# Performance work log

Measured on AMD Instinct MI355X. Metric: run time of the kernel, lower is better.

Reference implementation:

```python
import jax, jax.numpy as jnp
import numpy as np

B, N, E = 4, 2048, 512
H, DK, DV = 8, 64, 64
QKV_OUT = H * (2 * DK + DV)  # 1536


def setup_inputs() -> dict:
    key = jax.random.key(0)
    ks = jax.random.split(key, 5)
    s_in = 1.0 / np.sqrt(E)
    s_o = 1.0 / np.sqrt(H * DV)
    x = jax.random.normal(ks[0], (B, N, E), dtype=jnp.float32)
    W_qkv = jax.random.uniform(ks[1], (E, QKV_OUT), jnp.float32, -s_in, s_in)
    b_qkv = jax.random.uniform(ks[2], (QKV_OUT,), jnp.float32, -s_in, s_in)
    W_o = jax.random.uniform(ks[3], (H * DV, E), jnp.float32, -s_o, s_o)
    b_o = jax.random.uniform(ks[4], (E,), jnp.float32, -s_o, s_o)
    return {"x": x, "W_qkv": W_qkv, "b_qkv": b_qkv, "W_o": W_o, "b_o": b_o}


def reference(x, W_qkv, b_qkv, W_o, b_o):
    scale = DK ** (-0.5)
    qkv = x @ W_qkv + b_qkv                      # [B, N, H*(2dk+dv)]
    # Faithful to torch: raw view (B, H, N, 2dk+dv), NOT a head-split transpose.
    qkv = qkv.reshape(B, H, N, 2 * DK + DV)
    q = qkv[..., :DK]
    k = qkv[..., DK:2 * DK]
    v = qkv[..., 2 * DK:]
    # Faithful bug: qk /= scale with scale = dk^-0.5 -> multiply by sqrt(dk).
    qk = jnp.einsum('bhnd,bhmd->bhnm', q, k) / scale   # [B, H, N, N]
    attn = jax.nn.softmax(qk, axis=-1)
    y = jnp.einsum('bhnm,bhmd->bhnd', attn, v)         # [B, H, N, dv]
    y = y.reshape(B, N, H * DV)
    return y @ W_o + b_o
```

## Files before the change

kernel.cpp:

```cpp
#include <hip/hip_runtime.h>
#include <hip/hip_bf16.h>
#include <math.h>


typedef __attribute__((ext_vector_type(8))) short bf16x8;
typedef __attribute__((ext_vector_type(4))) float f32x4;

#define MFMA16(a, b, c) __builtin_amdgcn_mfma_f32_16x16x32_bf16((a), (b), (c), 0, 0, 0)

__device__ __forceinline__ ushort f2bf_rne(float f) {
  union { float f; unsigned u; } v; v.f = f;
  return (ushort)((v.u + 0x7fffu + ((v.u >> 16) & 1u)) >> 16);
}
__device__ __forceinline__ float bf2f(ushort h) {
  union { float f; unsigned u; } v; v.u = ((unsigned)h) << 16; return v.f;
}
__device__ __forceinline__ void split2(float f, ushort& hi, ushort& lo) {
  union { float f; unsigned u; } v; v.f = f;
  hi = (ushort)(v.u >> 16);
  union { float f; unsigned u; } r; r.f = f - bf2f(hi);
  lo = (ushort)(r.u >> 16);
}

__global__ __launch_bounds__(256) void cvtw_k(const float* __restrict__ wqkv,
                                              const float* __restrict__ wo,
                                              ushort* __restrict__ wT_hi,
                                              ushort* __restrict__ wT_lo,
                                              ushort* __restrict__ woT)
{
  const int gid = blockIdx.x * 256 + threadIdx.x;
  if (gid < 786432) {
    const int n = gid >> 9, k = gid & 511;
    ushort hi, lo; split2(wqkv[(size_t)k * 1536 + n], hi, lo);
    wT_hi[gid] = hi; wT_lo[gid] = lo;
  } else {
    const int g = gid - 786432;
    const int n = g >> 9, k = g & 511;
    woT[g] = f2bf_rne(wo[(size_t)k * 512 + n]);
  }
}

__global__ __launch_bounds__(256) void cvtx_k(const float* __restrict__ x,
                                              ushort* __restrict__ xh,
                                              ushort* __restrict__ xl)
{
  const int gid = blockIdx.x * 256 + threadIdx.x;
  float4 v = ((const float4*)x)[gid];
  ushort4 hh, ll;
  split2(v.x, hh.x, ll.x); split2(v.y, hh.y, ll.y);
  split2(v.z, hh.z, ll.z); split2(v.w, hh.w, ll.w);
  ((ushort4*)xh)[gid] = hh;
  ((ushort4*)xl)[gid] = ll;
}

template <bool PRECVT>
__global__ __launch_bounds__(256) void qkv_gemm_k(
    const float* __restrict__ x,
    const ushort* __restrict__ xh, const ushort* __restrict__ xl,
    const ushort* __restrict__ wT_hi, const ushort* __restrict__ wT_lo,
    const float* __restrict__ bqkv,
    ushort* __restrict__ q_hi, ushort* __restrict__ q_lo,
    ushort* __restrict__ k_hi, ushort* __restrict__ k_lo,
    ushort* __restrict__ v_nat)
{
  const int i = blockIdx.x, j = i >> 3;
  const int tmb = (i & 7) * 8 + (j & 7);
  const int tn  = j >> 3;
  const int tid = threadIdx.x, lane = tid & 63, w = tid >> 6;
  const int col16 = lane & 15, quad = lane >> 4;
  const int wr = w >> 1, wc = w & 1;

  __shared__ short bh_lds[2][128][40];
  __shared__ short bl_lds[2][128][40];

  const int sn = tid >> 1, sk = (tid & 1) * 16;
  const ushort* bhsrc = wT_hi + (size_t)(tn * 128 + sn) * 512 + sk;
  const ushort* blsrc = wT_lo + (size_t)(tn * 128 + sn) * 512 + sk;

  const float*  axf[4];
  const ushort *axh[4], *axl[4];
#pragma unroll
  for (int rt = 0; rt < 4; ++rt) {
    const size_t rowoff = (size_t)(tmb * 128 + wr * 64 + rt * 16 + col16) * 512 + quad * 8;
    axf[rt] = x  + rowoff;
    axh[rt] = xh + rowoff;
    axl[rt] = xl + rowoff;
  }

  f32x4 acc[4][4];
#pragma unroll
  for (int rt = 0; rt < 4; ++rt)
#pragma unroll
    for (int ct = 0; ct < 4; ++ct) acc[rt][ct] = (f32x4){0.f, 0.f, 0.f, 0.f};

  uint4 rb0 = *(const uint4*)(bhsrc);
  uint4 rb1 = *(const uint4*)(bhsrc + 8);
  uint4 rb2 = *(const uint4*)(blsrc);
  uint4 rb3 = *(const uint4*)(blsrc + 8);
  *(uint4*)(&bh_lds[0][sn][sk])     = rb0;
  *(uint4*)(&bh_lds[0][sn][sk + 8]) = rb1;
  *(uint4*)(&bl_lds[0][sn][sk])     = rb2;
  *(uint4*)(&bl_lds[0][sn][sk + 8]) = rb3;

  for (int c = 0; c < 16; ++c) {
    __syncthreads();
    if (c < 15) {
      const int k0 = (c + 1) * 32;
      rb0 = *(const uint4*)(bhsrc + k0);
      rb1 = *(const uint4*)(bhsrc + k0 + 8);
      rb2 = *(const uint4*)(blsrc + k0);
      rb3 = *(const uint4*)(blsrc + k0 + 8);
    }
    const int b = c & 1, k0 = c * 32;

    bf16x8 bh[4], bl[4];
#pragma unroll
    for (int ct = 0; ct < 4; ++ct) {
      bh[ct] = *(const bf16x8*)(&bh_lds[b][wc * 64 + ct * 16 + col16][quad * 8]);
      bl[ct] = *(const bf16x8*)(&bl_lds[b][wc * 64 + ct * 16 + col16][quad * 8]);
    }
#pragma unroll
    for (int rt = 0; rt < 4; ++rt) {
      bf16x8 a_hi, a_lo;
      if constexpr (PRECVT) {
        a_hi = *(const bf16x8*)(axh[rt] + k0);
        a_lo = *(const bf16x8*)(axl[rt] + k0);
      } else {
        float4 xa = *(const float4*)(axf[rt] + k0);
        float4 xb = *(const float4*)(axf[rt] + k0 + 4);
#pragma unroll
        for (int jj = 0; jj < 4; ++jj) {
          ushort h, l;
          split2(((const float*)&xa)[jj], h, l);
          ((short*)&a_hi)[jj] = (short)h; ((short*)&a_lo)[jj] = (short)l;
          split2(((const float*)&xb)[jj], h, l);
          ((short*)&a_hi)[4 + jj] = (short)h; ((short*)&a_lo)[4 + jj] = (short)l;
        }
      }
#pragma unroll
      for (int ct = 0; ct < 4; ++ct) {
        acc[rt][ct] = MFMA16(a_hi, bh[ct], acc[rt][ct]);
        acc[rt][ct] = MFMA16(a_hi, bl[ct], acc[rt][ct]);
        acc[rt][ct] = MFMA16(a_lo, bh[ct], acc[rt][ct]);
      }
    }
    if (c < 15) {
      const int nb = b ^ 1;
      *(uint4*)(&bh_lds[nb][sn][sk])     = rb0;
      *(uint4*)(&bh_lds[nb][sn][sk + 8]) = rb1;
      *(uint4*)(&bl_lds[nb][sn][sk])     = rb2;
      *(uint4*)(&bl_lds[nb][sn][sk + 8]) = rb3;
    }
  }

  short* eph = ((short*)bh_lds) + w * 1152;
  short* epl = ((short*)bl_lds) + w * 1152;
  const int g0   = tn * 128 + wc * 64;
  const int sect = (g0 % 192) >> 6;
  const int s    = g0 / 192;
  float bv[4];
#pragma unroll
  for (int ct = 0; ct < 4; ++ct) bv[ct] = bqkv[g0 + ct * 16 + col16];

#pragma unroll
  for (int rt = 0; rt < 4; ++rt) {
#pragma unroll
    for (int ct = 0; ct < 4; ++ct) {
#pragma unroll
      for (int r = 0; r < 4; ++r) {
        const float val = acc[rt][ct][r] + bv[ct];
        const int o = (quad * 4 + r) * 72 + ct * 16 + col16;
        if (sect == 2) {
          eph[o] = (short)f2bf_rne(val);
        } else {
          ushort h, l; split2(val, h, l);
          eph[o] = (short)h; epl[o] = (short)l;
        }
      }
    }
#pragma unroll
    for (int p = 0; p < 2; ++p) {
      const int row = p * 8 + (lane >> 3);
      const int dsg = (lane & 7) * 8;
      const int grow = tmb * 128 + wr * 64 + rt * 16 + row;
      const int bhh = grow >> 8, a = grow & 255;
      const size_t idx = ((size_t)bhh * 2048 + 8 * a + s) * 64 + dsg;
      uint4 hv = *(const uint4*)(eph + row * 72 + dsg);
      if (sect == 0) {
        *(uint4*)(q_hi + idx) = hv;
        uint4 lv = *(const uint4*)(epl + row * 72 + dsg);
        *(uint4*)(q_lo + idx) = lv;
      } else if (sect == 1) {
        *(uint4*)(k_hi + idx) = hv;
        uint4 lv = *(const uint4*)(epl + row * 72 + dsg);
        *(uint4*)(k_lo + idx) = lv;
      } else {
        *(uint4*)(v_nat + idx) = hv;
      }
    }
  }
}

__global__ __launch_bounds__(256) void vtrans_k(const ushort* __restrict__ v_nat,
                                                ushort* __restrict__ vT)
{
  const int t  = blockIdx.x & 7;
  const int bh = blockIdx.x >> 3;
  const int tid = threadIdx.x;
  const int nl = tid & 63;
  const int dg = tid >> 6;
  const size_t base = (size_t)bh * 2048 * 64;
#pragma unroll
  for (int p = 0; p < 2; ++p) {
    const int dseg = dg + p * 4;
#pragma unroll
    for (int nb = 0; nb < 4; ++nb) {
      const int n = t * 256 + nb * 64 + nl;
      uint4 vv = *(const uint4*)(v_nat + base + (size_t)n * 64 + dseg * 8);
      const ushort* pv = (const ushort*)&vv;
#pragma unroll
      for (int j = 0; j < 8; ++j)
        vT[base + (size_t)(dseg * 8 + j) * 2048 + n] = pv[j];
    }
  }
}

__global__ __launch_bounds__(256, 2) void attn_k(
    const ushort* __restrict__ q_hi, const ushort* __restrict__ q_lo,
    const ushort* __restrict__ k_hi, const ushort* __restrict__ k_lo,
    const ushort* __restrict__ vT, ushort* __restrict__ y)
{
  const int i  = blockIdx.x;
  const int bh = (i & 7) * 4 + (i >> 7);
  const int qt = (i >> 3) & 15;
  const int tid = threadIdx.x, lane = tid & 63, w = tid >> 6;
  const int col16 = lane & 15, quad = lane >> 4;

  __shared__ short kh_lds[2][64][72], kl_lds[2][64][72], vt_lds[2][64][72];
  __shared__ short p_lds[4][2][16][72];

  const size_t base = (size_t)bh * 2048 * 64;
  const int qw = qt * 128 + w * 32;

  bf16x8 qh[2][2], ql[2][2];
#pragma unroll
  for (int rf = 0; rf < 2; ++rf)
#pragma unroll
    for (int ks = 0; ks < 2; ++ks) {
      const size_t off = base + (size_t)(qw + rf * 16 + col16) * 64 + ks * 32 + quad * 8;
      qh[rf][ks] = *(const bf16x8*)(q_hi + off);
      ql[rf][ks] = *(const bf16x8*)(q_lo + off);
    }

  f32x4 oacc[2][4];
#pragma unroll
  for (int rf = 0; rf < 2; ++rf)
#pragma unroll
    for (int ct = 0; ct < 4; ++ct) oacc[rf][ct] = (f32x4){0.f, 0.f, 0.f, 0.f};
  f32x4 lsum[2] = {(f32x4){0.f, 0.f, 0.f, 0.f}, (f32x4){0.f, 0.f, 0.f, 0.f}};

  const int sn = tid >> 2, sd = (tid & 3) * 16;
  const ushort* khsrc = k_hi + base + (size_t)sn * 64 + sd;
  const ushort* klsrc = k_lo + base + (size_t)sn * 64 + sd;
  const ushort* vtsrc = vT  + base + (size_t)sn * 2048 + sd;

  const float S2 = 11.541560327111707f;

  uint4 r0 = *(const uint4*)(khsrc);
  uint4 r1 = *(const uint4*)(khsrc + 8);
  uint4 r2 = *(const uint4*)(klsrc);
  uint4 r3 = *(const uint4*)(klsrc + 8);
  uint4 r4 = *(const uint4*)(vtsrc);
  uint4 r5 = *(const uint4*)(vtsrc + 8);
  *(uint4*)(&kh_lds[0][sn][sd])     = r0;
  *(uint4*)(&kh_lds[0][sn][sd + 8]) = r1;
  *(uint4*)(&kl_lds[0][sn][sd])     = r2;
  *(uint4*)(&kl_lds[0][sn][sd + 8]) = r3;
  *(uint4*)(&vt_lds[0][sn][sd])     = r4;
  *(uint4*)(&vt_lds[0][sn][sd + 8]) = r5;

  for (int c = 0; c < 32; ++c) {
    __syncthreads();
    if (c < 31) {
      const size_t ko = (size_t)(c + 1) * 4096;
      r0 = *(const uint4*)(khsrc + ko);
      r1 = *(const uint4*)(khsrc + ko + 8);
      r2 = *(const uint4*)(klsrc + ko);
      r3 = *(const uint4*)(klsrc + ko + 8);
      r4 = *(const uint4*)(vtsrc + (c + 1) * 64);
      r5 = *(const uint4*)(vtsrc + (c + 1) * 64 + 8);
    }
    const int b = c & 1;

    f32x4 sacc[2][4];
#pragma unroll
    for (int rf = 0; rf < 2; ++rf)
#pragma unroll
      for (int ct = 0; ct < 4; ++ct) sacc[rf][ct] = (f32x4){0.f, 0.f, 0.f, 0.f};
#pragma unroll
    for (int ks = 0; ks < 2; ++ks) {
#pragma unroll
      for (int ct = 0; ct < 4; ++ct) {
        bf16x8 khf = *(const bf16x8*)(&kh_lds[b][ct * 16 + col16][ks * 32 + quad * 8]);
        bf16x8 klf = *(const bf16x8*)(&kl_lds[b][ct * 16 + col16][ks * 32 + quad * 8]);
#pragma unroll
        for (int rf = 0; rf < 2; ++rf) {
          sacc[rf][ct] = MFMA16(qh[rf][ks], khf, sacc[rf][ct]);
          sacc[rf][ct] = MFMA16(qh[rf][ks], klf, sacc[rf][ct]);
          sacc[rf][ct] = MFMA16(ql[rf][ks], khf, sacc[rf][ct]);
        }
      }
    }

#pragma unroll
    for (int rf = 0; rf < 2; ++rf) {
#pragma unroll
      for (int ct = 0; ct < 4; ++ct) {
#pragma unroll
        for (int r = 0; r < 4; ++r) {
          const float p = exp2f(fmaf(sacc[rf][ct][r], S2, -128.0f));
          union { float f; unsigned u; } pu; pu.f = p;
          union { unsigned u; float f; } pb; pb.u = pu.u & 0xffff0000u;
          lsum[rf][r] += pb.f;
          p_lds[w][rf][quad * 4 + r][ct * 16 + col16] = (short)(pu.u >> 16);
        }
      }
    }

#pragma unroll
    for (int ks = 0; ks < 2; ++ks) {
#pragma unroll
      for (int ct = 0; ct < 4; ++ct) {
        bf16x8 vv = *(const bf16x8*)(&vt_lds[b][ct * 16 + col16][ks * 32 + quad * 8]);
#pragma unroll
        for (int rf = 0; rf < 2; ++rf) {
          bf16x8 ap = *(const bf16x8*)(&p_lds[w][rf][col16][ks * 32 + quad * 8]);
          oacc[rf][ct] = MFMA16(ap, vv, oacc[rf][ct]);
        }
      }
    }

    if (c < 31) {
      const int nb = b ^ 1;
      *(uint4*)(&kh_lds[nb][sn][sd])     = r0;
      *(uint4*)(&kh_lds[nb][sn][sd + 8]) = r1;
      *(uint4*)(&kl_lds[nb][sn][sd])     = r2;
      *(uint4*)(&kl_lds[nb][sn][sd + 8]) = r3;
      *(uint4*)(&vt_lds[nb][sn][sd])     = r4;
      *(uint4*)(&vt_lds[nb][sn][sd + 8]) = r5;
    }
  }

#pragma unroll
  for (int rf = 0; rf < 2; ++rf) {
#pragma unroll
    for (int r = 0; r < 4; ++r) {
      float l = lsum[rf][r];
#pragma unroll
      for (int off = 1; off < 16; off <<= 1) l += __shfl_xor(l, off, 64);
      const float inv = 1.f / l;
      const int n = qw + rf * 16 + quad * 4 + r;
      const size_t orow = ((size_t)bh * 256 + (n >> 3)) * 512 + (n & 7) * 64;
#pragma unroll
      for (int ct = 0; ct < 4; ++ct)
        y[orow + ct * 16 + col16] = f2bf_rne(oacc[rf][ct][r] * inv);
    }
  }
}

__global__ __launch_bounds__(256) void out_gemm_k(
    const ushort* __restrict__ y, const ushort* __restrict__ woT,
    const float* __restrict__ bo, float* __restrict__ out)
{
  const int i = blockIdx.x, j = i >> 3;
  const int tmb = (i & 7) * 8 + (j & 7);
  const int tn  = j >> 3;
  const int tid = threadIdx.x, lane = tid & 63, w = tid >> 6;
  const int col16 = lane & 15, quad = lane >> 4;
  const int wr = w >> 1, wc = w & 1;

  __shared__ short b_lds[2][128][40];

  const int sn = tid >> 1, sk = (tid & 1) * 16;
  const ushort* bsrc = woT + (size_t)(tn * 128 + sn) * 512 + sk;

  const ushort* ay[4];
#pragma unroll
  for (int rt = 0; rt < 4; ++rt)
    ay[rt] = y + (size_t)(tmb * 128 + wr * 64 + rt * 16 + col16) * 512 + quad * 8;

  f32x4 acc[4][4];
#pragma unroll
  for (int rt = 0; rt < 4; ++rt)
#pragma unroll
    for (int ct = 0; ct < 4; ++ct) acc[rt][ct] = (f32x4){0.f, 0.f, 0.f, 0.f};

  uint4 rb0 = *(const uint4*)(bsrc);
  uint4 rb1 = *(const uint4*)(bsrc + 8);
  *(uint4*)(&b_lds[0][sn][sk])     = rb0;
  *(uint4*)(&b_lds[0][sn][sk + 8]) = rb1;

  for (int c = 0; c < 16; ++c) {
    __syncthreads();
    if (c < 15) {
      const int k0 = (c + 1) * 32;
      rb0 = *(const uint4*)(bsrc + k0);
      rb1 = *(const uint4*)(bsrc + k0 + 8);
    }
    const int b = c & 1, k0 = c * 32;
    bf16x8 bfr[4];
#pragma unroll
    for (int ct = 0; ct < 4; ++ct)
      bfr[ct] = *(const bf16x8*)(&b_lds[b][wc * 64 + ct * 16 + col16][quad * 8]);
#pragma unroll
    for (int rt = 0; rt < 4; ++rt) {
      bf16x8 af = *(const bf16x8*)(ay[rt] + k0);
#pragma unroll
      for (int ct = 0; ct < 4; ++ct)
        acc[rt][ct] = MFMA16(af, bfr[ct], acc[rt][ct]);
    }
    if (c < 15) {
      const int nb = b ^ 1;
      *(uint4*)(&b_lds[nb][sn][sk])     = rb0;
      *(uint4*)(&b_lds[nb][sn][sk + 8]) = rb1;
    }
  }
#pragma unroll
  for (int ct = 0; ct < 4; ++ct) {
    const int col = tn * 128 + wc * 64 + ct * 16 + col16;
    const float bval = bo[col];
#pragma unroll
    for (int rt = 0; rt < 4; ++rt) {
#pragma unroll
      for (int r = 0; r < 4; ++r) {
        const int row = tmb * 128 + wr * 64 + rt * 16 + quad * 4 + r;
        out[(size_t)row * 512 + col] = acc[rt][ct][r] + bval;
      }
    }
  }
}

extern "C" void kernel_launch(void* const* d_in, const int* in_sizes, int n_in,
                              void* d_out, int out_size, void* d_ws, size_t ws_size,
                              hipStream_t stream)
{
  const float* x    = (const float*)d_in[0];
  const float* Wqkv = (const float*)d_in[1];
  const float* bqkv = (const float*)d_in[2];
  const float* Wo   = (const float*)d_in[3];
  const float* bo   = (const float*)d_in[4];
  float* out = (float*)d_out;

  ushort* wT_hi = (ushort*)d_ws;
  ushort* wT_lo = wT_hi + 786432;
  ushort* woT   = wT_lo + 786432;
  ushort* q_hi  = woT   + 262144;
  ushort* q_lo  = q_hi  + 4194304;
  ushort* k_hi  = q_lo  + 4194304;
  ushort* k_lo  = k_hi  + 4194304;
  ushort* v_nat = k_lo  + 4194304;
  ushort* tail  = v_nat + 4194304;

  const bool roomy = ws_size >= 62390272ULL;
  ushort *xh, *xl, *vT, *y;
  if (roomy) {
    xh = tail; xl = tail + 4194304;
    vT = xh;   y  = xl;
  } else {
    xh = xl = nullptr;
    vT = tail; y = v_nat;
  }

  cvtw_k<<<4096, 256, 0, stream>>>(Wqkv, Wo, wT_hi, wT_lo, woT);
  if (roomy) {
    cvtx_k<<<4096, 256, 0, stream>>>(x, xh, xl);
    qkv_gemm_k<true><<<768, 256, 0, stream>>>(x, xh, xl, wT_hi, wT_lo, bqkv,
                                              q_hi, q_lo, k_hi, k_lo, v_nat);
  } else {
    qkv_gemm_k<false><<<768, 256, 0, stream>>>(x, nullptr, nullptr, wT_hi, wT_lo,
                                               bqkv, q_hi, q_lo, k_hi, k_lo, v_nat);
  }
  vtrans_k<<<256, 256, 0, stream>>>(v_nat, vT);
  attn_k<<<512, 256, 0, stream>>>(q_hi, q_lo, k_hi, k_lo, vT, y);
  out_gemm_k<<<256, 256, 0, stream>>>(y, woT, bo, out);
}
```

Measured before the change: 274.0 us.

## Split attention keys across waves with direct global loads and LDS reduction

The attention kernel moves from each wave owning 32 query rows to each block owning 64 query rows, with the four waves splitting the key range instead. K and V fragments are read straight from global memory rather than staged in double-buffered LDS, which removes the per-chunk barriers. Partial outputs and row sums are reduced across waves through LDS at the end, and the grid doubles to 1024 blocks. The costs are more global/L2 traffic for K and V, more accumulator registers per wave, and an extra reduction phase with barriers.

```diff
diff --git a/kernel.cpp b/kernel.cpp
--- a/kernel.cpp
+++ b/kernel.cpp
@@ -231,140 +231,126 @@
     const ushort* __restrict__ vT, ushort* __restrict__ y)
 {
   const int i  = blockIdx.x;
-  const int bh = (i & 7) * 4 + (i >> 7);
-  const int qt = (i >> 3) & 15;
+  const int bh = (i & 7) * 4 + (i >> 8);
+  const int qt = (i >> 3) & 31;
   const int tid = threadIdx.x, lane = tid & 63, w = tid >> 6;
   const int col16 = lane & 15, quad = lane >> 4;
 
-  __shared__ short kh_lds[2][64][72], kl_lds[2][64][72], vt_lds[2][64][72];
-  __shared__ short p_lds[4][2][16][72];
+  __shared__ short p_lds[4][4][16][40];
+  __shared__ float red [4][16][68];
+  __shared__ float lred[4][16];
 
   const size_t base = (size_t)bh * 2048 * 64;
-  const int qw = qt * 128 + w * 32;
-
-  bf16x8 qh[2][2], ql[2][2];
-#pragma unroll
-  for (int rf = 0; rf < 2; ++rf)
+  const int qb = qt * 64;
+
+  bf16x8 qh[4][2], ql[4][2];
+#pragma unroll
+  for (int rf = 0; rf < 4; ++rf)
 #pragma unroll
     for (int ks = 0; ks < 2; ++ks) {
-      const size_t off = base + (size_t)(qw + rf * 16 + col16) * 64 + ks * 32 + quad * 8;
+      const size_t off = base + (size_t)(qb + rf * 16 + col16) * 64 + ks * 32 + quad * 8;
       qh[rf][ks] = *(const bf16x8*)(q_hi + off);
       ql[rf][ks] = *(const bf16x8*)(q_lo + off);
     }
 
-  f32x4 oacc[2][4];
-#pragma unroll
-  for (int rf = 0; rf < 2; ++rf)
+  f32x4 oacc[4][4];
+#pragma unroll
+  for (int rf = 0; rf < 4; ++rf)
 #pragma unroll
     for (int ct = 0; ct < 4; ++ct) oacc[rf][ct] = (f32x4){0.f, 0.f, 0.f, 0.f};
-  f32x4 lsum[2] = {(f32x4){0.f, 0.f, 0.f, 0.f}, (f32x4){0.f, 0.f, 0.f, 0.f}};
-
-  const int sn = tid >> 2, sd = (tid & 3) * 16;
-  const ushort* khsrc = k_hi + base + (size_t)sn * 64 + sd;
-  const ushort* klsrc = k_lo + base + (size_t)sn * 64 + sd;
-  const ushort* vtsrc = vT  + base + (size_t)sn * 2048 + sd;
+  f32x4 lsum[4];
+#pragma unroll
+  for (int rf = 0; rf < 4; ++rf) lsum[rf] = (f32x4){0.f, 0.f, 0.f, 0.f};
 
   const float S2 = 11.541560327111707f;
 
-  uint4 r0 = *(const uint4*)(khsrc);
-  uint4 r1 = *(const uint4*)(khsrc + 8);
-  uint4 r2 = *(const uint4*)(klsrc);
-  uint4 r3 = *(const uint4*)(klsrc + 8);
-  uint4 r4 = *(const uint4*)(vtsrc);
-  uint4 r5 = *(const uint4*)(vtsrc + 8);
-  *(uint4*)(&kh_lds[0][sn][sd])     = r0;
-  *(uint4*)(&kh_lds[0][sn][sd + 8]) = r1;
-  *(uint4*)(&kl_lds[0][sn][sd])     = r2;
-  *(uint4*)(&kl_lds[0][sn][sd + 8]) = r3;
-  *(uint4*)(&vt_lds[0][sn][sd])     = r4;
-  *(uint4*)(&vt_lds[0][sn][sd + 8]) = r5;
-
-  for (int c = 0; c < 32; ++c) {
-    __syncthreads();
-    if (c < 31) {
-      const size_t ko = (size_t)(c + 1) * 4096;
-      r0 = *(const uint4*)(khsrc + ko);
-      r1 = *(const uint4*)(khsrc + ko + 8);
-      r2 = *(const uint4*)(klsrc + ko);
-      r3 = *(const uint4*)(klsrc + ko + 8);
-      r4 = *(const uint4*)(vtsrc + (c + 1) * 64);
-      r5 = *(const uint4*)(vtsrc + (c + 1) * 64 + 8);
-    }
-    const int b = c & 1;
-
-    f32x4 sacc[2][4];
-#pragma unroll
-    for (int rf = 0; rf < 2; ++rf)
-#pragma unroll
-      for (int ct = 0; ct < 4; ++ct) sacc[rf][ct] = (f32x4){0.f, 0.f, 0.f, 0.f};
-#pragma unroll
-    for (int ks = 0; ks < 2; ++ks) {
-#pragma unroll
-      for (int ct = 0; ct < 4; ++ct) {
-        bf16x8 khf = *(const bf16x8*)(&kh_lds[b][ct * 16 + col16][ks * 32 + quad * 8]);
-        bf16x8 klf = *(const bf16x8*)(&kl_lds[b][ct * 16 + col16][ks * 32 + quad * 8]);
-#pragma unroll
-        for (int rf = 0; rf < 2; ++rf) {
-          sacc[rf][ct] = MFMA16(qh[rf][ks], khf, sacc[rf][ct]);
-          sacc[rf][ct] = MFMA16(qh[rf][ks], klf, sacc[rf][ct]);
-          sacc[rf][ct] = MFMA16(ql[rf][ks], khf, sacc[rf][ct]);
+  for (int it = 0; it < 16; ++it) {
+    const int kb = it * 128 + w * 32;
+
+    bf16x8 vf[4];
+#pragma unroll
+    for (int ct = 0; ct < 4; ++ct)
+      vf[ct] = *(const bf16x8*)(vT + base + (size_t)(ct * 16 + col16) * 2048 + kb + quad * 8);
+
+#pragma unroll
+    for (int kt = 0; kt < 2; ++kt) {
+      bf16x8 khf[2], klf[2];
+#pragma unroll
+      for (int ks = 0; ks < 2; ++ks) {
+        const size_t off = base + (size_t)(kb + kt * 16 + col16) * 64 + ks * 32 + quad * 8;
+        khf[ks] = *(const bf16x8*)(k_hi + off);
+        klf[ks] = *(const bf16x8*)(k_lo + off);
+      }
+      f32x4 sacc[4];
+#pragma unroll
+      for (int rf = 0; rf < 4; ++rf) sacc[rf] = (f32x4){0.f, 0.f, 0.f, 0.f};
+#pragma unroll
+      for (int ks = 0; ks < 2; ++ks)
+#pragma unroll
+        for (int rf = 0; rf < 4; ++rf) {
+          sacc[rf] = MFMA16(qh[rf][ks], khf[ks], sacc[rf]);
+          sacc[rf] = MFMA16(qh[rf][ks], klf[ks], sacc[rf]);
+          sacc[rf] = MFMA16(ql[rf][ks], khf[ks], sacc[rf]);
         }
-      }
-    }
-
-#pragma unroll
-    for (int rf = 0; rf < 2; ++rf) {
-#pragma unroll
-      for (int ct = 0; ct < 4; ++ct) {
+#pragma unroll
+      for (int rf = 0; rf < 4; ++rf)
 #pragma unroll
         for (int r = 0; r < 4; ++r) {
-          const float p = exp2f(fmaf(sacc[rf][ct][r], S2, -128.0f));
+          const float p = exp2f(fmaf(sacc[rf][r], S2, -128.0f));
           union { float f; unsigned u; } pu; pu.f = p;
           union { unsigned u; float f; } pb; pb.u = pu.u & 0xffff0000u;
           lsum[rf][r] += pb.f;
-          p_lds[w][rf][quad * 4 + r][ct * 16 + col16] = (short)(pu.u >> 16);
+          p_lds[w][rf][quad * 4 + r][kt * 16 + col16] = (short)(pu.u >> 16);
         }
-      }
-    }
-
-#pragma unroll
-    for (int ks = 0; ks < 2; ++ks) {
-#pragma unroll
-      for (int ct = 0; ct < 4; ++ct) {
-        bf16x8 vv = *(const bf16x8*)(&vt_lds[b][ct * 16 + col16][ks * 32 + quad * 8]);
-#pragma unroll
-        for (int rf = 0; rf < 2; ++rf) {
-          bf16x8 ap = *(const bf16x8*)(&p_lds[w][rf][col16][ks * 32 + quad * 8]);
-          oacc[rf][ct] = MFMA16(ap, vv, oacc[rf][ct]);
-        }
-      }
-    }
-
-    if (c < 31) {
-      const int nb = b ^ 1;
-      *(uint4*)(&kh_lds[nb][sn][sd])     = r0;
-      *(uint4*)(&kh_lds[nb][sn][sd + 8]) = r1;
-      *(uint4*)(&kl_lds[nb][sn][sd])     = r2;
-      *(uint4*)(&kl_lds[nb][sn][sd + 8]) = r3;
-      *(uint4*)(&vt_lds[nb][sn][sd])     = r4;
-      *(uint4*)(&vt_lds[nb][sn][sd + 8]) = r5;
-    }
-  }
-
-#pragma unroll
-  for (int rf = 0; rf < 2; ++rf) {
+    }
+
+#pragma unroll
+    for (int rf = 0; rf < 4; ++rf) {
+      bf16x8 apf = *(const bf16x8*)(&p_lds[w][rf][col16][quad * 8]);
+#pragma unroll
+      for (int ct = 0; ct < 4; ++ct)
+        oacc[rf][ct] = MFMA16(apf, vf[ct], oacc[rf][ct]);
+    }
+  }
+
+#pragma unroll
+  for (int rf = 0; rf < 4; ++rf) {
+    if (rf) __syncthreads();
+    float lrow[4];
 #pragma unroll
     for (int r = 0; r < 4; ++r) {
       float l = lsum[rf][r];
 #pragma unroll
       for (int off = 1; off < 16; off <<= 1) l += __shfl_xor(l, off, 64);
-      const float inv = 1.f / l;
-      const int n = qw + rf * 16 + quad * 4 + r;
-      const size_t orow = ((size_t)bh * 256 + (n >> 3)) * 512 + (n & 7) * 64;
-#pragma unroll
-      for (int ct = 0; ct < 4; ++ct)
-        y[orow + ct * 16 + col16] = f2bf_rne(oacc[rf][ct][r] * inv);
-    }
+      lrow[r] = l;
+    }
+    if (col16 == 0) {
+#pragma unroll
+      for (int r = 0; r < 4; ++r) lred[w][quad * 4 + r] = lrow[r];
+    }
+#pragma unroll
+    for (int ct = 0; ct < 4; ++ct)
+#pragma unroll
+      for (int r = 0; r < 4; ++r)
+        red[w][quad * 4 + r][ct * 16 + col16] = oacc[rf][ct][r];
+    __syncthreads();
+
+    const int row = tid >> 4, db = (tid & 15) * 4;
+    f32x4 s = (f32x4){0.f, 0.f, 0.f, 0.f};
+    float l = 0.f;
+#pragma unroll
+    for (int ww = 0; ww < 4; ++ww) {
+      const f32x4 t = *(const f32x4*)(&red[ww][row][db]);
+      s += t;
+      l += lred[ww][row];
+    }
+    const float inv = 1.f / l;
+    const int n = qb + rf * 16 + row;
+    const size_t orow = ((size_t)bh * 256 + (n >> 3)) * 512 + (n & 7) * 64 + db;
+    ushort4 o4;
+    o4.x = f2bf_rne(s[0] * inv); o4.y = f2bf_rne(s[1] * inv);
+    o4.z = f2bf_rne(s[2] * inv); o4.w = f2bf_rne(s[3] * inv);
+    *(ushort4*)(y + orow) = o4;
   }
 }
 
@@ -481,6 +467,6 @@
                                                bqkv, q_hi, q_lo, k_hi, k_lo, v_nat);
   }
   vtrans_k<<<256, 256, 0, stream>>>(v_nat, vT);
-  attn_k<<<512, 256, 0, stream>>>(q_hi, q_lo, k_hi, k_lo, vT, y);
+  attn_k<<<1024, 256, 0, stream>>>(q_hi, q_lo, k_hi, k_lo, vT, y);
   out_gemm_k<<<256, 256, 0, stream>>>(y, woT, bo, out);
 }
```

New measurement: 287.1 us. 1.05x slower.
